# Performance work log

Hardware: AMD Instinct MI355X
Metric: run time of the kernel (lower is better)

The kernel has to match this reference:

```python
import jax, jax.numpy as jnp
import numpy as np

N_NODES = 10000
N_EDGES = 160000
N_IN, H, HEADS, HOUT = 128, 256, 2, 256
BATCH_SIZE = 8192


def setup_inputs() -> dict:
    key = jax.random.key(0)
    ks = jax.random.split(key, 20)
    s = 0.05
    inp = {
        "x": jax.random.normal(ks[0], (N_NODES, N_IN), dtype=jnp.float32),
        "edge_index": jax.random.randint(ks[1], (2, N_EDGES), 0, N_NODES, dtype=jnp.int64),
        "batch_size": BATCH_SIZE,
        # encoder: Linear(128,256), LayerNorm(256), ReLU, Linear(256,256)
        "enc_w1": jax.random.normal(ks[2], (H, N_IN), dtype=jnp.float32) * s,
        "enc_b1": jnp.zeros((H,), jnp.float32),
        "ln_g": jnp.ones((H,), jnp.float32),
        "ln_b": jnp.zeros((H,), jnp.float32),
        "enc_w2": jax.random.normal(ks[3], (H, H), dtype=jnp.float32) * s,
        "enc_b2": jnp.zeros((H,), jnp.float32),
        # GATConv(256, 256, heads=2): lin 256->512 (no bias), att vectors, out bias [512]
        "gat_w": jax.random.normal(ks[4], (HEADS * HOUT, H), dtype=jnp.float32) * s,
        "att_src": jax.random.normal(ks[5], (HEADS, HOUT), dtype=jnp.float32) * s,
        "att_dst": jax.random.normal(ks[6], (HEADS, HOUT), dtype=jnp.float32) * s,
        "gat_bias": jnp.zeros((HEADS * HOUT,), jnp.float32),
        # skip: Linear(256, 512)
        "skip_w": jax.random.normal(ks[7], (HEADS * HOUT, H), dtype=jnp.float32) * s,
        "skip_b": jnp.zeros((HEADS * HOUT,), jnp.float32),
        # decoder: Linear(512,1024) -> LeakyReLU(0.1) -> Linear(1024,1)
        "dec_w1": jax.random.normal(ks[8], (4 * H, HEADS * HOUT), dtype=jnp.float32) * s,
        "dec_b1": jnp.zeros((4 * H,), jnp.float32),
        "dec_w2": jax.random.normal(ks[9], (1, 4 * H), dtype=jnp.float32) * s,
        "dec_b2": jnp.zeros((1,), jnp.float32),
    }
    return inp


def _elu(x, alpha):
    return jnp.where(x > 0, x, alpha * (jnp.exp(x) - 1.0))


def _leaky(x, slope):
    return jnp.where(x > 0, x, slope * x)


def _forward(x, edge_index, batch_size, enc_w1, enc_b1, ln_g, ln_b, enc_w2, enc_b2,
             gat_w, att_src, att_dst, gat_bias, skip_w, skip_b,
             dec_w1, dec_b1, dec_w2, dec_b2):
    n = x.shape[0]
    # encoder
    h = x @ enc_w1.T + enc_b1
    mu = jnp.mean(h, axis=-1, keepdims=True)
    var = jnp.mean((h - mu) ** 2, axis=-1, keepdims=True)
    h = (h - mu) * jax.lax.rsqrt(var + 1e-5) * ln_g + ln_b
    h = jax.nn.relu(h)
    h = h @ enc_w2.T + enc_b2  # [N, 256]

    # GATConv with self-loops (PyG default add_self_loops=True)
    loops = jnp.arange(n, dtype=edge_index.dtype)
    src = jnp.concatenate([edge_index[0], loops])
    tgt = jnp.concatenate([edge_index[1], loops])

    xs = (h @ gat_w.T).reshape(n, HEADS, HOUT)  # [N, heads, out]
    a_src = jnp.sum(xs * att_src[None], axis=-1)  # [N, heads]
    a_dst = jnp.sum(xs * att_dst[None], axis=-1)  # [N, heads]

    e = _leaky(a_src[src] + a_dst[tgt], 0.2)  # [E', heads]
    m = jax.ops.segment_max(e, tgt, num_segments=n)
    w = jnp.exp(e - m[tgt])
    z = jax.ops.segment_sum(w, tgt, num_segments=n)
    alpha = w / z[tgt]  # [E', heads]

    msg = xs[src] * alpha[:, :, None]  # [E', heads, out]
    agg = jax.ops.segment_sum(msg, tgt, num_segments=n).reshape(n, HEADS * HOUT)
    conv = agg + gat_bias

    out = conv + h @ skip_w.T + skip_b
    out = _elu(out, 0.1)  # ELU(alpha=0.1)

    # decoder
    d = _leaky(out @ dec_w1.T + dec_b1, 0.1)
    y = d @ dec_w2.T + dec_b2
    return y[:batch_size]


def reference(x, edge_index, batch_size, enc_w1, enc_b1, ln_g, ln_b, enc_w2, enc_b2,
              gat_w, att_src, att_dst, gat_bias, skip_w, skip_b,
              dec_w1, dec_b1, dec_w2, dec_b2):
    return _forward(x, edge_index, batch_size, enc_w1, enc_b1, ln_g, ln_b, enc_w2, enc_b2,
                    gat_w, att_src, att_dst, gat_bias, skip_w, skip_b,
                    dec_w1, dec_b1, dec_w2, dec_b2)
```

## Files before the change

### kernel.cpp

```cpp
#include <hip/hip_runtime.h>


#define N_NODES  10000
#define N_EDGES  160000
#define E_TOT    (N_EDGES + N_NODES)
#define NBATCH   8192
#define DIM_IN   128
#define DIM_H    256
#define DIM_GAT  512
#define DIM_DEC  1024
#define MPAD     10112

typedef short bf16x8 __attribute__((ext_vector_type(8)));
typedef float f32x4  __attribute__((ext_vector_type(4)));

__device__ __forceinline__ ushort f2bf(float f) {
    union { float f; unsigned u; } c; c.f = f;
    unsigned u = c.u + 0x7FFFu + ((c.u >> 16) & 1u);
    return (ushort)(u >> 16);
}
__device__ __forceinline__ float bf2f(ushort h) {
    union { unsigned u; float f; } c; c.u = ((unsigned)h) << 16; return c.f;
}

template<int BM, int BN, int BK, int TM, int TN>
__global__ __launch_bounds__(256)
void gemm_kernel(const float* __restrict__ A, const float* __restrict__ W,
                 const float* __restrict__ bias, float* __restrict__ C,
                 int M, int N, int K)
{
    constexpr int TX = BN / TN;
    constexpr int TY = BM / TM;
    static_assert(TX * TY == 256, "block must be 256 threads");
    __shared__ float As[BK][BM + 4];
    __shared__ float Ws[BK][BN + 4];

    const int tid = threadIdx.x;
    const int tx  = tid % TX;
    const int ty  = tid / TX;
    const int bm  = blockIdx.x * BM;
    const int bn  = blockIdx.y * BN;

    float acc[TM][TN];
    #pragma unroll
    for (int i = 0; i < TM; ++i)
        #pragma unroll
        for (int j = 0; j < TN; ++j) acc[i][j] = 0.f;

    constexpr int A_LOADS = BM * BK / 4 / 256;
    constexpr int W_LOADS = BN * BK / 4 / 256;
    constexpr int KQ = BK / 4;

    for (int k0 = 0; k0 < K; k0 += BK) {
        #pragma unroll
        for (int l = 0; l < A_LOADS; ++l) {
            int idx = tid + l * 256, row = idx / KQ, kq = idx % KQ;
            int grow = bm + row;
            float4 v = make_float4(0.f, 0.f, 0.f, 0.f);
            if (grow < M)
                v = *reinterpret_cast<const float4*>(&A[(size_t)grow * K + k0 + kq * 4]);
            As[kq * 4 + 0][row] = v.x; As[kq * 4 + 1][row] = v.y;
            As[kq * 4 + 2][row] = v.z; As[kq * 4 + 3][row] = v.w;
        }
        #pragma unroll
        for (int l = 0; l < W_LOADS; ++l) {
            int idx = tid + l * 256, row = idx / KQ, kq = idx % KQ;
            float4 v = *reinterpret_cast<const float4*>(&W[(size_t)(bn + row) * K + k0 + kq * 4]);
            Ws[kq * 4 + 0][row] = v.x; Ws[kq * 4 + 1][row] = v.y;
            Ws[kq * 4 + 2][row] = v.z; Ws[kq * 4 + 3][row] = v.w;
        }
        __syncthreads();
        #pragma unroll
        for (int kk = 0; kk < BK; ++kk) {
            float af[TM], wf[TN];
            #pragma unroll
            for (int i = 0; i < TM; ++i) af[i] = As[kk][ty * TM + i];
            #pragma unroll
            for (int j = 0; j < TN; ++j) wf[j] = Ws[kk][tx * TN + j];
            #pragma unroll
            for (int i = 0; i < TM; ++i)
                #pragma unroll
                for (int j = 0; j < TN; ++j)
                    acc[i][j] = fmaf(af[i], wf[j], acc[i][j]);
        }
        __syncthreads();
    }

    #pragma unroll
    for (int i = 0; i < TM; ++i) {
        int grow = bm + ty * TM + i;
        if (grow < M) {
            #pragma unroll
            for (int j = 0; j < TN; ++j) {
                int gcol = bn + tx * TN + j;
                C[(size_t)grow * N + gcol] = acc[i][j] + bias[gcol];
            }
        }
    }
}

__device__ __forceinline__ void stage_tile(ushort* T, const ushort* __restrict__ G,
                                           int rowbase, int K, int k0, int tid, int wv)
{
    #pragma unroll
    for (int i = 0; i < 4; ++i) {
        int m   = i * 32 + (tid >> 3);
        int scb = ((tid & 7) << 4) ^ ((m & 7) << 4);
        const char* gsrc = (const char*)G + ((size_t)(rowbase + m) * K + k0) * 2 + scb;
        char* ldst = (char*)T + i * 4096 + wv * 1024;
        __builtin_amdgcn_global_load_lds(
            (const __attribute__((address_space(1))) void*)gsrc,
            (__attribute__((address_space(3))) void*)ldst, 16, 0, 0);
    }
}

__device__ __forceinline__ bf16x8 ldfrag(const ushort* T, int row, int kcb)
{
    int addr = (row << 7) + (kcb ^ ((row & 7) << 4));
    return *reinterpret_cast<const bf16x8*>(reinterpret_cast<const char*>(T) + addr);
}

template<int EPI>
__global__ __launch_bounds__(256, 2)
void mgemm(const ushort* __restrict__ Ah, const ushort* __restrict__ Al,
           const ushort* __restrict__ Wh, const ushort* __restrict__ Wl,
           const float* __restrict__ bias, const float* __restrict__ bias2,
           const float* __restrict__ addmat, float* __restrict__ outF,
           ushort* __restrict__ outHi, ushort* __restrict__ outLo,
           const float* __restrict__ w2, const float* __restrict__ b2,
           float* __restrict__ yout, int M, int N, int K)
{
    __shared__ __align__(16) ushort tAh[8192];
    __shared__ __align__(16) ushort tAl[8192];
    __shared__ __align__(16) ushort tWh[8192];
    __shared__ __align__(16) ushort tWl[8192];

    const int tid    = threadIdx.x;
    const int lane   = tid & 63;
    const int wv     = tid >> 6;
    const int wr     = wv >> 1, wc = wv & 1;
    const int bm     = blockIdx.x * 128;
    const int bn     = blockIdx.y * 128;
    const int lane15 = lane & 15;
    const int kgrp16 = (lane >> 4) << 4;
    const int r0     = (lane >> 4) << 2;

    f32x4 acc[4][4];
    const f32x4 zero = {0.f, 0.f, 0.f, 0.f};
    #pragma unroll
    for (int i = 0; i < 4; ++i)
        #pragma unroll
        for (int j = 0; j < 4; ++j) acc[i][j] = zero;

    for (int k0 = 0; k0 < K; k0 += 64) {
        stage_tile(tAh, Ah, bm, K, k0, tid, wv);
        stage_tile(tAl, Al, bm, K, k0, tid, wv);
        stage_tile(tWh, Wh, bn, K, k0, tid, wv);
        stage_tile(tWl, Wl, bn, K, k0, tid, wv);
        __syncthreads();
        #pragma unroll
        for (int kk = 0; kk < 2; ++kk) {
            const int kcb = kk * 64 + kgrp16;
            bf16x8 ah[4], al[4], wh[4], wl[4];
            #pragma unroll
            for (int f = 0; f < 4; ++f) {
                ah[f] = ldfrag(tAh, wr * 64 + f * 16 + lane15, kcb);
                al[f] = ldfrag(tAl, wr * 64 + f * 16 + lane15, kcb);
                wh[f] = ldfrag(tWh, wc * 64 + f * 16 + lane15, kcb);
                wl[f] = ldfrag(tWl, wc * 64 + f * 16 + lane15, kcb);
            }
            #pragma unroll
            for (int fm = 0; fm < 4; ++fm)
                #pragma unroll
                for (int fn = 0; fn < 4; ++fn) {
                    acc[fm][fn] = __builtin_amdgcn_mfma_f32_16x16x32_bf16(ah[fm], wh[fn], acc[fm][fn], 0, 0, 0);
                    acc[fm][fn] = __builtin_amdgcn_mfma_f32_16x16x32_bf16(ah[fm], wl[fn], acc[fm][fn], 0, 0, 0);
                    acc[fm][fn] = __builtin_amdgcn_mfma_f32_16x16x32_bf16(al[fm], wh[fn], acc[fm][fn], 0, 0, 0);
                }
        }
        __syncthreads();
    }

    if (EPI != 3) {
        #pragma unroll
        for (int fm = 0; fm < 4; ++fm) {
            #pragma unroll
            for (int r = 0; r < 4; ++r) {
                int row = bm + wr * 64 + fm * 16 + r0 + r;
                if (row < M) {
                    #pragma unroll
                    for (int fn = 0; fn < 4; ++fn) {
                        int col = bn + wc * 64 + fn * 16 + lane15;
                        float v = acc[fm][fn][r];
                        if (EPI == 1 || EPI == 2) v += bias[col];
                        if (EPI == 2) {
                            v += bias2[col] + addmat[(size_t)row * N + col];
                            v = v > 0.f ? v : 0.1f * (expf(v) - 1.f);
                        }
                        if (EPI == 0) {
                            outF[(size_t)row * N + col] = v;
                        } else {
                            ushort h = f2bf(v);
                            outHi[(size_t)row * N + col] = h;
                            outLo[(size_t)row * N + col] = f2bf(v - bf2f(h));
                        }
                    }
                }
            }
        }
    } else {
        #pragma unroll
        for (int fm = 0; fm < 4; ++fm) {
            #pragma unroll
            for (int r = 0; r < 4; ++r) {
                int row = bm + wr * 64 + fm * 16 + r0 + r;
                float part = 0.f;
                #pragma unroll
                for (int fn = 0; fn < 4; ++fn) {
                    int col = bn + wc * 64 + fn * 16 + lane15;
                    float v = acc[fm][fn][r] + bias[col];
                    v = v > 0.f ? v : 0.1f * v;
                    part = fmaf(v, w2[col], part);
                }
                part += __shfl_xor(part, 1);
                part += __shfl_xor(part, 2);
                part += __shfl_xor(part, 4);
                part += __shfl_xor(part, 8);
                if (lane15 == 0 && row < M) {
                    float add = part + ((blockIdx.y == 0 && wc == 0) ? b2[0] : 0.f);
                    atomicAdd(&yout[row], add);
                }
            }
        }
    }
}

__global__ __launch_bounds__(256)
void split_kernel(const float* __restrict__ src, ushort* __restrict__ hi,
                  ushort* __restrict__ lo, int n)
{
    int i = blockIdx.x * 256 + threadIdx.x;
    if (i < n) {
        float v = src[i];
        ushort h = f2bf(v);
        hi[i] = h;
        lo[i] = f2bf(v - bf2f(h));
    }
}

__global__ void detect_kernel(const int* __restrict__ ei32, int* __restrict__ eflag)
{
    if (blockIdx.x == 0 && threadIdx.x == 0) {
        int s = 0;
        #pragma unroll
        for (int i = 0; i < 64; ++i) s |= ei32[2 * i + 1];
        eflag[0] = (s == 0) ? 2 : 1;
    }
}

__global__ __launch_bounds__(256)
void ln_relu_split_kernel(const float* __restrict__ h1, const float* __restrict__ g,
                          const float* __restrict__ b, ushort* __restrict__ hi,
                          ushort* __restrict__ lo)
{
    int wave = threadIdx.x >> 6, lane = threadIdx.x & 63;
    int row = blockIdx.x * 4 + wave;
    if (row >= N_NODES) return;
    float4 v = *reinterpret_cast<const float4*>(&h1[(size_t)row * DIM_H + lane * 4]);
    float s  = v.x + v.y + v.z + v.w;
    float sq = v.x * v.x + v.y * v.y + v.z * v.z + v.w * v.w;
    #pragma unroll
    for (int m = 1; m <= 32; m <<= 1) { s += __shfl_xor(s, m); sq += __shfl_xor(sq, m); }
    float mu  = s * (1.0f / 256.0f);
    float var = sq * (1.0f / 256.0f) - mu * mu;
    float rs  = 1.0f / sqrtf(var + 1e-5f);
    float4 gg = *reinterpret_cast<const float4*>(&g[lane * 4]);
    float4 bb = *reinterpret_cast<const float4*>(&b[lane * 4]);
    float o[4];
    o[0] = fmaxf((v.x - mu) * rs * gg.x + bb.x, 0.f);
    o[1] = fmaxf((v.y - mu) * rs * gg.y + bb.y, 0.f);
    o[2] = fmaxf((v.z - mu) * rs * gg.z + bb.z, 0.f);
    o[3] = fmaxf((v.w - mu) * rs * gg.w + bb.w, 0.f);
    ushort4 vh, vl;
    ushort* ph = &vh.x; ushort* pl = &vl.x;
    #pragma unroll
    for (int q = 0; q < 4; ++q) {
        ushort hh = f2bf(o[q]);
        ph[q] = hh;
        pl[q] = f2bf(o[q] - bf2f(hh));
    }
    *reinterpret_cast<ushort4*>(&hi[(size_t)row * DIM_H + lane * 4]) = vh;
    *reinterpret_cast<ushort4*>(&lo[(size_t)row * DIM_H + lane * 4]) = vl;
}

__global__ __launch_bounds__(256)
void attn_coef_kernel(const float* __restrict__ xs,
                      const float* __restrict__ att_src,
                      const float* __restrict__ att_dst,
                      float* __restrict__ asrc, float* __restrict__ adst)
{
    int wave = threadIdx.x >> 6, lane = threadIdx.x & 63;
    int node = blockIdx.x * 4 + wave;
    if (node >= N_NODES) return;
    const float4* xr = reinterpret_cast<const float4*>(&xs[(size_t)node * DIM_GAT + lane * 8]);
    const float4* sr = reinterpret_cast<const float4*>(&att_src[lane * 8]);
    const float4* dr = reinterpret_cast<const float4*>(&att_dst[lane * 8]);
    float ss = 0.f, sd = 0.f;
    #pragma unroll
    for (int q = 0; q < 2; ++q) {
        float4 a = xr[q], s = sr[q], d = dr[q];
        ss += a.x * s.x + a.y * s.y + a.z * s.z + a.w * s.w;
        sd += a.x * d.x + a.y * d.y + a.z * d.z + a.w * d.w;
    }
    #pragma unroll
    for (int m = 1; m <= 16; m <<= 1) { ss += __shfl_xor(ss, m); sd += __shfl_xor(sd, m); }
    if ((lane & 31) == 0) {
        int hh = lane >> 5;
        asrc[node * 2 + hh] = ss;
        adst[node * 2 + hh] = sd;
    }
}

__global__ __launch_bounds__(256)
void edge_w_kernel(const int* __restrict__ ei, const int* __restrict__ eflag,
                   const float* __restrict__ asrc, const float* __restrict__ adst,
                   float* __restrict__ wbuf, float* __restrict__ zbuf,
                   int* __restrict__ counts)
{
    int e = blockIdx.x * 256 + threadIdx.x;
    if (e >= E_TOT) return;
    const int stride = eflag[0];
    int src, tgt;
    if (e < N_EDGES) {
        src = ei[(size_t)stride * e];
        tgt = ei[(size_t)stride * (N_EDGES + e)];
    } else {
        src = tgt = e - N_EDGES;
    }
    #pragma unroll
    for (int hh = 0; hh < 2; ++hh) {
        float v = asrc[src * 2 + hh] + adst[tgt * 2 + hh];
        v = v > 0.f ? v : 0.2f * v;
        float w = expf(v);
        wbuf[e * 2 + hh] = w;
        atomicAdd(&zbuf[tgt * 2 + hh], w);
    }
    atomicAdd(&counts[tgt], 1);
}

__global__ __launch_bounds__(1024)
void scan_kernel(const int* __restrict__ counts, int* __restrict__ rowst)
{
    __shared__ int part[1024];
    const int t = threadIdx.x;
    const int base = t * 10;
    int loc[10];
    int s = 0;
    #pragma unroll
    for (int i = 0; i < 10; ++i) {
        int idx = base + i;
        int v = (idx < N_NODES) ? counts[idx] : 0;
        loc[i] = s;
        s += v;
    }
    part[t] = s;
    __syncthreads();
    for (int off = 1; off < 1024; off <<= 1) {
        int v = (t >= off) ? part[t - off] : 0;
        __syncthreads();
        part[t] += v;
        __syncthreads();
    }
    int chunk_excl = part[t] - s;
    #pragma unroll
    for (int i = 0; i < 10; ++i) {
        int idx = base + i;
        if (idx <= N_NODES) rowst[idx] = chunk_excl + loc[i];
    }
}

__global__ __launch_bounds__(256)
void scatter_kernel(const int* __restrict__ ei, const int* __restrict__ eflag,
                    const int* __restrict__ rowst,
                    int* __restrict__ cursor, unsigned int* __restrict__ ebuf)
{
    int e = blockIdx.x * 256 + threadIdx.x;
    if (e >= E_TOT) return;
    const int stride = eflag[0];
    int src, tgt;
    if (e < N_EDGES) {
        src = ei[(size_t)stride * e];
        tgt = ei[(size_t)stride * (N_EDGES + e)];
    } else {
        src = tgt = e - N_EDGES;
    }
    int pos = atomicAdd(&cursor[tgt], 1);
    ebuf[rowst[tgt] + pos] = ((unsigned int)e << 14) | (unsigned int)src;
}

__global__ __launch_bounds__(256)
void agg_kernel(const float* __restrict__ xs,
                const float* __restrict__ wbuf, const float* __restrict__ zbuf,
                const int* __restrict__ rowst, const unsigned int* __restrict__ ebuf,
                float* __restrict__ agg)
{
    int n = blockIdx.x;
    int t = threadIdx.x;
    float inv0 = 1.0f / zbuf[n * 2 + 0];
    float inv1 = 1.0f / zbuf[n * 2 + 1];
    float acc0 = 0.f, acc1 = 0.f;
    int beg = rowst[n], end = rowst[n + 1];
    for (int j = beg; j < end; ++j) {
        unsigned int pk = ebuf[j];
        int e   = (int)(pk >> 14);
        int src = (int)(pk & 0x3FFFu);
        float a0 = wbuf[e * 2 + 0] * inv0;
        float a1 = wbuf[e * 2 + 1] * inv1;
        const float* xr = &xs[(size_t)src * DIM_GAT];
        acc0 = fmaf(xr[t], a0, acc0);
        acc1 = fmaf(xr[256 + t], a1, acc1);
    }
    agg[(size_t)n * DIM_GAT + t]       = acc0;
    agg[(size_t)n * DIM_GAT + 256 + t] = acc1;
}

extern "C" void kernel_launch(void* const* d_in, const int* in_sizes, int n_in,
                              void* d_out, int out_size, void* d_ws, size_t ws_size,
                              hipStream_t stream)
{
    const float* x        = (const float*)d_in[0];
    const int*   ei       = (const int*)  d_in[1];
    const float* enc_w1   = (const float*)d_in[3];
    const float* enc_b1   = (const float*)d_in[4];
    const float* ln_g     = (const float*)d_in[5];
    const float* ln_b     = (const float*)d_in[6];
    const float* enc_w2   = (const float*)d_in[7];
    const float* enc_b2   = (const float*)d_in[8];
    const float* gat_w    = (const float*)d_in[9];
    const float* att_src  = (const float*)d_in[10];
    const float* att_dst  = (const float*)d_in[11];
    const float* gat_bias = (const float*)d_in[12];
    const float* skip_w   = (const float*)d_in[13];
    const float* skip_b   = (const float*)d_in[14];
    const float* dec_w1   = (const float*)d_in[15];
    const float* dec_b1   = (const float*)d_in[16];
    const float* dec_w2   = (const float*)d_in[17];
    const float* dec_b2   = (const float*)d_in[18];
    float* y = (float*)d_out;

    float* ws = (float*)d_ws;
    float*  h1      = ws;
    ushort* h1ln_hi = (ushort*)(ws + 2560000);
    ushort* h1ln_lo = h1ln_hi + (size_t)MPAD * DIM_H;
    float*  xs      = ws;
    ushort* outb_hi = (ushort*)ws;
    ushort* outb_lo = outb_hi + (size_t)NBATCH * DIM_GAT;
    ushort* h_hi = (ushort*)(ws + 5242880);
    ushort* h_lo = h_hi + (size_t)MPAD * DIM_H;
    float* agg = ws + 7842880;
    ushort* wsp = (ushort*)(ws + 12037184);
    ushort* w2h = wsp;
    ushort* w2l = w2h + 65536;
    ushort* gwh = w2l + 65536;
    ushort* gwl = gwh + 131072;
    ushort* swh = gwl + 131072;
    ushort* swl = swh + 131072;
    ushort* d1h = swl + 131072;
    ushort* d1l = d1h + 524288;
    float* S      = ws + 12889152;
    float* asrc   = S;
    float* adst   = S + 20000;
    float* wbuf   = S + 40000;
    float* zbuf   = S + 380000;
    int*   counts = (int*)(S + 400000);
    int*   cursor = counts + 10000;
    int*   rowst  = cursor + 10000;
    unsigned int* ebuf = (unsigned int*)(rowst + 10001);
    int*   eflag  = (int*)(ebuf + 170000);

    hipMemsetAsync(zbuf, 0, 40000 * sizeof(float), stream);
    hipMemsetAsync(y, 0, (size_t)NBATCH * sizeof(float), stream);
    detect_kernel<<<1, 1, 0, stream>>>(ei, eflag);

    split_kernel<<<256,  256, 0, stream>>>(enc_w2, w2h, w2l, 65536);
    split_kernel<<<512,  256, 0, stream>>>(gat_w,  gwh, gwl, 131072);
    split_kernel<<<512,  256, 0, stream>>>(skip_w, swh, swl, 131072);
    split_kernel<<<2048, 256, 0, stream>>>(dec_w1, d1h, d1l, 524288);

    gemm_kernel<64, 64, 16, 4, 4><<<dim3(157, 4), 256, 0, stream>>>(
        x, enc_w1, enc_b1, h1, N_NODES, DIM_H, DIM_IN);
    ln_relu_split_kernel<<<2500, 256, 0, stream>>>(h1, ln_g, ln_b, h1ln_hi, h1ln_lo);
    mgemm<1><<<dim3(79, 2), 256, 0, stream>>>(
        h1ln_hi, h1ln_lo, w2h, w2l, enc_b2, nullptr, nullptr,
        nullptr, h_hi, h_lo, nullptr, nullptr, nullptr, N_NODES, DIM_H, DIM_H);
    mgemm<0><<<dim3(79, 4), 256, 0, stream>>>(
        h_hi, h_lo, gwh, gwl, nullptr, nullptr, nullptr,
        xs, nullptr, nullptr, nullptr, nullptr, nullptr, N_NODES, DIM_GAT, DIM_H);
    attn_coef_kernel<<<2500, 256, 0, stream>>>(xs, att_src, att_dst, asrc, adst);
    edge_w_kernel<<<(E_TOT + 255) / 256, 256, 0, stream>>>(
        ei, eflag, asrc, adst, wbuf, zbuf, counts);
    scan_kernel<<<1, 1024, 0, stream>>>(counts, rowst);
    scatter_kernel<<<(E_TOT + 255) / 256, 256, 0, stream>>>(
        ei, eflag, rowst, cursor, ebuf);
    agg_kernel<<<NBATCH, 256, 0, stream>>>(xs, wbuf, zbuf, rowst, ebuf, agg);
    mgemm<2><<<dim3(64, 4), 256, 0, stream>>>(
        h_hi, h_lo, swh, swl, skip_b, gat_bias, agg,
        nullptr, outb_hi, outb_lo, nullptr, nullptr, nullptr, NBATCH, DIM_GAT, DIM_H);
    mgemm<3><<<dim3(64, 8), 256, 0, stream>>>(
        outb_hi, outb_lo, d1h, d1l, dec_b1, nullptr, nullptr,
        nullptr, nullptr, nullptr, dec_w2, dec_b2, y, NBATCH, DIM_DEC, DIM_GAT);
}
```

Baseline: 296.7 us.

## Fuse attention coefficients into GAT GEMM epilogue and store xs as bf16

The GAT projection GEMM epilogue now computes the per-node att_src and att_dst dot products with shuffle reductions and atomicAdd, which removes the separate attn_coef kernel and its full fp32 reread of xs. xs is stored as bf16 instead of fp32, halving its write and the gather traffic in agg_kernel. agg_kernel is restructured to handle two columns per thread for a single head, with the edge loop unrolled by four. The cost is lower precision of the aggregated features and atomics on the coefficient buffers, which now need zeroing.

```diff
diff --git a/kernel.cpp b/kernel.cpp
--- a/kernel.cpp
+++ b/kernel.cpp
@@ -128,6 +128,7 @@
            const float* __restrict__ addmat, float* __restrict__ outF,
            ushort* __restrict__ outHi, ushort* __restrict__ outLo,
            const float* __restrict__ w2, const float* __restrict__ b2,
+           float* __restrict__ aS, float* __restrict__ aD,
            float* __restrict__ yout, int M, int N, int K)
 {
     __shared__ __align__(16) ushort tAh[8192];
@@ -181,7 +182,35 @@
         __syncthreads();
     }
 
-    if (EPI != 3) {
+    if (EPI == 0) {
+        const int head = bn >> 8;
+        #pragma unroll
+        for (int fm = 0; fm < 4; ++fm) {
+            #pragma unroll
+            for (int r = 0; r < 4; ++r) {
+                int row = bm + wr * 64 + fm * 16 + r0 + r;
+                if (row < M) {
+                    float sp = 0.f, dp = 0.f;
+                    #pragma unroll
+                    for (int fn = 0; fn < 4; ++fn) {
+                        int col = bn + wc * 64 + fn * 16 + lane15;
+                        float v = acc[fm][fn][r];
+                        outHi[(size_t)row * N + col] = f2bf(v);
+                        sp = fmaf(v, bias[col], sp);
+                        dp = fmaf(v, bias2[col], dp);
+                    }
+                    sp += __shfl_xor(sp, 1); sp += __shfl_xor(sp, 2);
+                    sp += __shfl_xor(sp, 4); sp += __shfl_xor(sp, 8);
+                    dp += __shfl_xor(dp, 1); dp += __shfl_xor(dp, 2);
+                    dp += __shfl_xor(dp, 4); dp += __shfl_xor(dp, 8);
+                    if (lane15 == 0) {
+                        atomicAdd(&aS[row * 2 + head], sp);
+                        atomicAdd(&aD[row * 2 + head], dp);
+                    }
+                }
+            }
+        }
+    } else if (EPI == 1 || EPI == 2) {
         #pragma unroll
         for (int fm = 0; fm < 4; ++fm) {
             #pragma unroll
@@ -191,19 +220,14 @@
                     #pragma unroll
                     for (int fn = 0; fn < 4; ++fn) {
                         int col = bn + wc * 64 + fn * 16 + lane15;
-                        float v = acc[fm][fn][r];
-                        if (EPI == 1 || EPI == 2) v += bias[col];
+                        float v = acc[fm][fn][r] + bias[col];
                         if (EPI == 2) {
                             v += bias2[col] + addmat[(size_t)row * N + col];
                             v = v > 0.f ? v : 0.1f * (expf(v) - 1.f);
                         }
-                        if (EPI == 0) {
-                            outF[(size_t)row * N + col] = v;
-                        } else {
-                            ushort h = f2bf(v);
-                            outHi[(size_t)row * N + col] = h;
-                            outLo[(size_t)row * N + col] = f2bf(v - bf2f(h));
-                        }
+                        ushort h = f2bf(v);
+                        outHi[(size_t)row * N + col] = h;
+                        outLo[(size_t)row * N + col] = f2bf(v - bf2f(h));
                     }
                 }
             }
@@ -294,34 +318,6 @@
 }
 
 __global__ __launch_bounds__(256)
-void attn_coef_kernel(const float* __restrict__ xs,
-                      const float* __restrict__ att_src,
-                      const float* __restrict__ att_dst,
-                      float* __restrict__ asrc, float* __restrict__ adst)
-{
-    int wave = threadIdx.x >> 6, lane = threadIdx.x & 63;
-    int node = blockIdx.x * 4 + wave;
-    if (node >= N_NODES) return;
-    const float4* xr = reinterpret_cast<const float4*>(&xs[(size_t)node * DIM_GAT + lane * 8]);
-    const float4* sr = reinterpret_cast<const float4*>(&att_src[lane * 8]);
-    const float4* dr = reinterpret_cast<const float4*>(&att_dst[lane * 8]);
-    float ss = 0.f, sd = 0.f;
-    #pragma unroll
-    for (int q = 0; q < 2; ++q) {
-        float4 a = xr[q], s = sr[q], d = dr[q];
-        ss += a.x * s.x + a.y * s.y + a.z * s.z + a.w * s.w;
-        sd += a.x * d.x + a.y * d.y + a.z * d.z + a.w * d.w;
-    }
-    #pragma unroll
-    for (int m = 1; m <= 16; m <<= 1) { ss += __shfl_xor(ss, m); sd += __shfl_xor(sd, m); }
-    if ((lane & 31) == 0) {
-        int hh = lane >> 5;
-        asrc[node * 2 + hh] = ss;
-        adst[node * 2 + hh] = sd;
-    }
-}
-
-__global__ __launch_bounds__(256)
 void edge_w_kernel(const int* __restrict__ ei, const int* __restrict__ eflag,
                    const float* __restrict__ asrc, const float* __restrict__ adst,
                    float* __restrict__ wbuf, float* __restrict__ zbuf,
@@ -399,29 +395,45 @@
 }
 
 __global__ __launch_bounds__(256)
-void agg_kernel(const float* __restrict__ xs,
+void agg_kernel(const ushort* __restrict__ xs_b,
                 const float* __restrict__ wbuf, const float* __restrict__ zbuf,
                 const int* __restrict__ rowst, const unsigned int* __restrict__ ebuf,
                 float* __restrict__ agg)
 {
-    int n = blockIdx.x;
-    int t = threadIdx.x;
-    float inv0 = 1.0f / zbuf[n * 2 + 0];
-    float inv1 = 1.0f / zbuf[n * 2 + 1];
+    const int n = blockIdx.x;
+    const int t = threadIdx.x;
+    const int h = t >> 7;
+    const float inv = 1.0f / zbuf[n * 2 + h];
     float acc0 = 0.f, acc1 = 0.f;
-    int beg = rowst[n], end = rowst[n + 1];
-    for (int j = beg; j < end; ++j) {
-        unsigned int pk = ebuf[j];
-        int e   = (int)(pk >> 14);
-        int src = (int)(pk & 0x3FFFu);
-        float a0 = wbuf[e * 2 + 0] * inv0;
-        float a1 = wbuf[e * 2 + 1] * inv1;
-        const float* xr = &xs[(size_t)src * DIM_GAT];
-        acc0 = fmaf(xr[t], a0, acc0);
-        acc1 = fmaf(xr[256 + t], a1, acc1);
-    }
-    agg[(size_t)n * DIM_GAT + t]       = acc0;
-    agg[(size_t)n * DIM_GAT + 256 + t] = acc1;
+    const int beg = rowst[n], end = rowst[n + 1];
+    int j = beg;
+    for (; j + 3 < end; j += 4) {
+        unsigned pk0 = ebuf[j],     pk1 = ebuf[j + 1];
+        unsigned pk2 = ebuf[j + 2], pk3 = ebuf[j + 3];
+        float w0 = wbuf[(pk0 >> 14) * 2 + h];
+        float w1 = wbuf[(pk1 >> 14) * 2 + h];
+        float w2 = wbuf[(pk2 >> 14) * 2 + h];
+        float w3 = wbuf[(pk3 >> 14) * 2 + h];
+        ushort2 x0 = *reinterpret_cast<const ushort2*>(&xs_b[(size_t)(pk0 & 0x3FFFu) * DIM_GAT + 2 * t]);
+        ushort2 x1 = *reinterpret_cast<const ushort2*>(&xs_b[(size_t)(pk1 & 0x3FFFu) * DIM_GAT + 2 * t]);
+        ushort2 x2 = *reinterpret_cast<const ushort2*>(&xs_b[(size_t)(pk2 & 0x3FFFu) * DIM_GAT + 2 * t]);
+        ushort2 x3 = *reinterpret_cast<const ushort2*>(&xs_b[(size_t)(pk3 & 0x3FFFu) * DIM_GAT + 2 * t]);
+        float a0 = w0 * inv, a1 = w1 * inv, a2 = w2 * inv, a3 = w3 * inv;
+        acc0 = fmaf(bf2f(x0.x), a0, acc0); acc1 = fmaf(bf2f(x0.y), a0, acc1);
+        acc0 = fmaf(bf2f(x1.x), a1, acc0); acc1 = fmaf(bf2f(x1.y), a1, acc1);
+        acc0 = fmaf(bf2f(x2.x), a2, acc0); acc1 = fmaf(bf2f(x2.y), a2, acc1);
+        acc0 = fmaf(bf2f(x3.x), a3, acc0); acc1 = fmaf(bf2f(x3.y), a3, acc1);
+    }
+    for (; j < end; ++j) {
+        unsigned pk = ebuf[j];
+        float w = wbuf[(pk >> 14) * 2 + h];
+        ushort2 x = *reinterpret_cast<const ushort2*>(&xs_b[(size_t)(pk & 0x3FFFu) * DIM_GAT + 2 * t]);
+        float a = w * inv;
+        acc0 = fmaf(bf2f(x.x), a, acc0);
+        acc1 = fmaf(bf2f(x.y), a, acc1);
+    }
+    agg[(size_t)n * DIM_GAT + 2 * t]     = acc0;
+    agg[(size_t)n * DIM_GAT + 2 * t + 1] = acc1;
 }
 
 extern "C" void kernel_launch(void* const* d_in, const int* in_sizes, int n_in,
@@ -452,7 +464,7 @@
     float*  h1      = ws;
     ushort* h1ln_hi = (ushort*)(ws + 2560000);
     ushort* h1ln_lo = h1ln_hi + (size_t)MPAD * DIM_H;
-    float*  xs      = ws;
+    ushort* xs_b    = (ushort*)ws;
     ushort* outb_hi = (ushort*)ws;
     ushort* outb_lo = outb_hi + (size_t)NBATCH * DIM_GAT;
     ushort* h_hi = (ushort*)(ws + 5242880);
@@ -470,15 +482,15 @@
     float* S      = ws + 12889152;
     float* asrc   = S;
     float* adst   = S + 20000;
-    float* wbuf   = S + 40000;
-    float* zbuf   = S + 380000;
-    int*   counts = (int*)(S + 400000);
+    float* zbuf   = S + 40000;
+    int*   counts = (int*)(S + 60000);
     int*   cursor = counts + 10000;
-    int*   rowst  = cursor + 10000;
+    float* wbuf   = S + 80000;
+    int*   rowst  = (int*)(S + 420000);
     unsigned int* ebuf = (unsigned int*)(rowst + 10001);
     int*   eflag  = (int*)(ebuf + 170000);
 
-    hipMemsetAsync(zbuf, 0, 40000 * sizeof(float), stream);
+    hipMemsetAsync(asrc, 0, 80000 * sizeof(float), stream);
     hipMemsetAsync(y, 0, (size_t)NBATCH * sizeof(float), stream);
     detect_kernel<<<1, 1, 0, stream>>>(ei, eflag);
 
@@ -492,21 +504,24 @@
     ln_relu_split_kernel<<<2500, 256, 0, stream>>>(h1, ln_g, ln_b, h1ln_hi, h1ln_lo);
     mgemm<1><<<dim3(79, 2), 256, 0, stream>>>(
         h1ln_hi, h1ln_lo, w2h, w2l, enc_b2, nullptr, nullptr,
-        nullptr, h_hi, h_lo, nullptr, nullptr, nullptr, N_NODES, DIM_H, DIM_H);
+        nullptr, h_hi, h_lo, nullptr, nullptr, nullptr, nullptr, nullptr,
+        N_NODES, DIM_H, DIM_H);
     mgemm<0><<<dim3(79, 4), 256, 0, stream>>>(
-        h_hi, h_lo, gwh, gwl, nullptr, nullptr, nullptr,
-        xs, nullptr, nullptr, nullptr, nullptr, nullptr, N_NODES, DIM_GAT, DIM_H);
-    attn_coef_kernel<<<2500, 256, 0, stream>>>(xs, att_src, att_dst, asrc, adst);
+        h_hi, h_lo, gwh, gwl, att_src, att_dst, nullptr,
+        nullptr, xs_b, nullptr, nullptr, nullptr, asrc, adst, nullptr,
+        N_NODES, DIM_GAT, DIM_H);
     edge_w_kernel<<<(E_TOT + 255) / 256, 256, 0, stream>>>(
         ei, eflag, asrc, adst, wbuf, zbuf, counts);
     scan_kernel<<<1, 1024, 0, stream>>>(counts, rowst);
     scatter_kernel<<<(E_TOT + 255) / 256, 256, 0, stream>>>(
         ei, eflag, rowst, cursor, ebuf);
-    agg_kernel<<<NBATCH, 256, 0, stream>>>(xs, wbuf, zbuf, rowst, ebuf, agg);
+    agg_kernel<<<NBATCH, 256, 0, stream>>>(xs_b, wbuf, zbuf, rowst, ebuf, agg);
     mgemm<2><<<dim3(64, 4), 256, 0, stream>>>(
         h_hi, h_lo, swh, swl, skip_b, gat_bias, agg,
-        nullptr, outb_hi, outb_lo, nullptr, nullptr, nullptr, NBATCH, DIM_GAT, DIM_H);
+        nullptr, outb_hi, outb_lo, nullptr, nullptr, nullptr, nullptr, nullptr,
+        NBATCH, DIM_GAT, DIM_H);
     mgemm<3><<<dim3(64, 8), 256, 0, stream>>>(
         outb_hi, outb_lo, d1h, d1l, dec_b1, nullptr, nullptr,
-        nullptr, nullptr, nullptr, dec_w2, dec_b2, y, NBATCH, DIM_DEC, DIM_GAT);
-}
+        nullptr, nullptr, nullptr, dec_w2, dec_b2, nullptr, nullptr, y,
+        NBATCH, DIM_DEC, DIM_GAT);
+}
```

Result: faster. 275.7 us (-7.1%).
